# Optimization experiments

Measured on AMD Instinct MI355X. Metric: run time of the kernel, lower is better.

Reference implementation:

```python
import jax, jax.numpy as jnp
import numpy as np

WS = 512            # window_size
STEP = WS // 2      # hop
K = WS // 2 + 1     # rfft coeffs = 257


def hann(n):
    # periodic hann window (matches torch.hann_window default)
    return 0.5 * (1.0 - jnp.cos(2.0 * jnp.pi * jnp.arange(n) / n))


def setup_inputs() -> dict:
    key = jax.random.key(0)
    k1, k2, k3 = jax.random.split(key, 3)
    B, C, T = 4, 64, 65536
    x = jax.random.normal(k1, (B, C, T), dtype=jnp.float32)
    # mixer initialized near identity (nn.Parameter(torch.eye(C)) after some training)
    mixer = jnp.eye(C, dtype=jnp.float32) + 0.01 * jax.random.normal(k2, (C, C), dtype=jnp.float32)
    # stable per-coefficient transfer magnitudes in [0, 0.9)
    transfer = jax.random.uniform(k3, (C, K), dtype=jnp.float32) * 0.9
    gain = jnp.full((1,), 1.5, dtype=jnp.float32)
    return {"x": x, "mixer": mixer, "transfer": transfer, "gain": gain}


def reference(x, mixer, transfer, gain):
    B, C, T = x.shape
    # (x^T @ mixer)^T
    x = jnp.einsum('bct,cd->bdt', x, mixer)
    # windowed_audio: pad by hop, unfold into half-overlapping frames
    xp = jnp.pad(x, ((0, 0), (0, 0), (0, STEP)))
    n_frames = (xp.shape[-1] - WS) // STEP + 1
    idx = jnp.arange(n_frames)[:, None] * STEP + jnp.arange(WS)[None, :]  # [F, WS]
    windowed = xp[:, :, idx]                     # [B, C, F, WS]
    spec = jnp.fft.rfft(windowed, axis=-1)       # [B, C, F, K] complex64
    # linear recurrence over frames: y_i = (spec_i + y_{i-1}) * transfer
    def step(carry, s):
        y = (s + carry) * transfer[None]         # [B, C, K]
        return y, y
    spec_t = jnp.transpose(spec, (2, 0, 1, 3))   # [F, B, C, K]
    y0 = jnp.zeros((B, C, K), dtype=spec.dtype)
    _, ys = jax.lax.scan(step, y0, spec_t)       # [F, B, C, K]
    out_spec = jnp.transpose(ys, (1, 2, 0, 3))   # [B, C, F, K]
    # inverse FFT + windowed overlap-add
    aw = jnp.fft.irfft(out_spec, n=WS, axis=-1)  # [B, C, F, WS]
    aw = aw * hann(WS)[None, None, None, :]
    L = (n_frames - 1) * STEP + WS
    samples = jnp.zeros((B, C, L), dtype=aw.dtype).at[:, :, idx].add(aw)
    samples = jnp.tanh(samples * gain[0])
    return samples[..., :T]
```

## Files before the change

kernel.cpp:

```cpp
#include <hip/hip_runtime.h>
#include <math.h>

#define T_LEN  65536
#define T_PAD  65792
#define C_CH   64
#define STEP_  256
#define K_     257
#define NW     16
#define NIT    16
#define SPEC_ROW  257
#define SPEC_ROWF (2 * SPEC_ROW)

#define PIDX8(i) ((i) + (((i) >> 3) << 1))

#define WSYNC()  asm volatile("s_waitcnt lgkmcnt(0)" ::: "memory")
#define CFENCE() asm volatile("" ::: "memory")

__device__ __forceinline__ float2 cadd(float2 a, float2 b) { return make_float2(a.x + b.x, a.y + b.y); }
__device__ __forceinline__ float2 csub(float2 a, float2 b) { return make_float2(a.x - b.x, a.y - b.y); }
__device__ __forceinline__ float2 cmul(float2 a, float2 b) {
    return make_float2(a.x * b.x - a.y * b.y, a.x * b.y + a.y * b.x);
}
template <int SGN>
__device__ __forceinline__ float2 cmulsg(float2 w, float2 t) {
    if (SGN > 0) return make_float2(w.x * t.x - w.y * t.y, w.x * t.y + w.y * t.x);
    else         return make_float2(w.x * t.x + w.y * t.y, w.x * t.y - w.y * t.x);
}

template <int SGN>
__device__ __forceinline__ void bfly4(float2 z0, float2 z1, float2 z2, float2 z3,
                                      float2& o0, float2& o1, float2& o2, float2& o3,
                                      float2 w1, float2 w2, float2 w3) {
    float2 apc = cadd(z0, z2), amc = csub(z0, z2);
    float2 bpd = cadd(z1, z3), bmd = csub(z1, z3);
    float2 jb  = make_float2(-bmd.y, bmd.x);
    float2 t1, t3;
    if (SGN > 0) { t1 = csub(amc, jb); t3 = cadd(amc, jb); }
    else         { t1 = cadd(amc, jb); t3 = csub(amc, jb); }
    o0 = cadd(apc, bpd);
    o1 = cmulsg<SGN>(w1, t1);
    o2 = cmulsg<SGN>(w2, csub(apc, bpd));
    o3 = cmulsg<SGN>(w3, t3);
}
template <int SGN>
__device__ __forceinline__ void bfly4nt(float2 z0, float2 z1, float2 z2, float2 z3,
                                        float2& o0, float2& o1, float2& o2, float2& o3) {
    float2 apc = cadd(z0, z2), amc = csub(z0, z2);
    float2 bpd = cadd(z1, z3), bmd = csub(z1, z3);
    float2 jb  = make_float2(-bmd.y, bmd.x);
    o0 = cadd(apc, bpd);
    o2 = csub(apc, bpd);
    if (SGN > 0) { o1 = csub(amc, jb); o3 = cadd(amc, jb); }
    else         { o1 = cadd(amc, jb); o3 = csub(amc, jb); }
}

__device__ __forceinline__ float ftanh(float x) {
    float e = __expf(2.0f * x);
    return 1.0f - 2.0f * __builtin_amdgcn_rcpf(e + 1.0f);
}

__global__ __launch_bounds__(512, 1) void mix_kernel(const float* __restrict__ x,
                                                     const float* __restrict__ mixer,
                                                     float* __restrict__ mixed) {
    __shared__ __align__(16) float xt[64][128];
    __shared__ __align__(16) float mx[64][64];
    int tid = threadIdx.x;
    int b   = blockIdx.y;
    int t0  = blockIdx.x * 128;

    if (t0 >= T_LEN) {
        for (int f = tid; f < 8192; f += 512) {
            int d = f >> 7, tt = f & 127;
            mixed[((size_t)(b * C_CH + d)) * T_PAD + t0 + tt] = 0.0f;
        }
        return;
    }
    for (int f = tid; f < 4096; f += 512) reinterpret_cast<float*>(mx)[f] = mixer[f];
    for (int f4 = tid; f4 < 2048; f4 += 512) {
        int cc = f4 >> 5, tt4 = f4 & 31;
        *reinterpret_cast<float4*>(&xt[cc][tt4 * 4]) =
            *reinterpret_cast<const float4*>(&x[((size_t)(b * C_CH + cc)) * T_LEN + t0 + tt4 * 4]);
    }
    __syncthreads();

    int t = tid & 127, w = tid >> 7;
    int dbase = w * 16;
    float acc[16];
#pragma unroll
    for (int i = 0; i < 16; ++i) acc[i] = 0.0f;
    for (int cc = 0; cc < 64; ++cc) {
        float xv = xt[cc][t];
        float4 m0 = *reinterpret_cast<const float4*>(&mx[cc][dbase + 0]);
        float4 m1 = *reinterpret_cast<const float4*>(&mx[cc][dbase + 4]);
        float4 m2 = *reinterpret_cast<const float4*>(&mx[cc][dbase + 8]);
        float4 m3 = *reinterpret_cast<const float4*>(&mx[cc][dbase + 12]);
        acc[0]  = fmaf(xv, m0.x, acc[0]);  acc[1]  = fmaf(xv, m0.y, acc[1]);
        acc[2]  = fmaf(xv, m0.z, acc[2]);  acc[3]  = fmaf(xv, m0.w, acc[3]);
        acc[4]  = fmaf(xv, m1.x, acc[4]);  acc[5]  = fmaf(xv, m1.y, acc[5]);
        acc[6]  = fmaf(xv, m1.z, acc[6]);  acc[7]  = fmaf(xv, m1.w, acc[7]);
        acc[8]  = fmaf(xv, m2.x, acc[8]);  acc[9]  = fmaf(xv, m2.y, acc[9]);
        acc[10] = fmaf(xv, m2.z, acc[10]); acc[11] = fmaf(xv, m2.w, acc[11]);
        acc[12] = fmaf(xv, m3.x, acc[12]); acc[13] = fmaf(xv, m3.y, acc[13]);
        acc[14] = fmaf(xv, m3.z, acc[14]); acc[15] = fmaf(xv, m3.w, acc[15]);
    }
#pragma unroll
    for (int i = 0; i < 16; ++i)
        mixed[((size_t)(b * C_CH + dbase + i)) * T_PAD + t0 + t] = acc[i];
}

__global__ __launch_bounds__(1024) void stft_kernel(const float* __restrict__ mixed,
                                                    const float* __restrict__ transfer,
                                                    const float* __restrict__ gainp,
                                                    float* __restrict__ out) {
    __shared__ __align__(16) float2 buf[NW][320];
    __shared__ __align__(16) float2 spec[NW][SPEC_ROW];
    __shared__ __align__(16) float  olab[NW][264];
    __shared__ __align__(16) float  tails[2][264];

    const int tid  = threadIdx.x;
    const int bc   = blockIdx.x;
    const int b    = bc >> 6, c = bc & 63;
    const int g    = tid >> 6, lane = tid & 63;

    const float* src = mixed + ((size_t)(b * C_CH + c)) * T_PAD;
    float*       dst = out   + ((size_t)(b * C_CH + c)) * T_LEN;

    float2 pf0, pf1, pf2, pf3;
    {
        const float* fp = src + (size_t)g * STEP_;
        pf0 = *reinterpret_cast<const float2*>(fp + 2 * lane);
        pf1 = *reinterpret_cast<const float2*>(fp + 2 * (lane + 64));
        pf2 = *reinterpret_cast<const float2*>(fp + 2 * (lane + 128));
        pf3 = *reinterpret_cast<const float2*>(fp + 2 * (lane + 192));
    }

    const float TWO_PI = 6.2831853071795864f;
    float sn, cn;
    sincosf(TWO_PI * (float)lane / 256.0f, &sn, &cn);
    float2 w1a = make_float2(cn, -sn), w2a = cmul(w1a, w1a), w3a = cmul(w2a, w1a);
    sincosf(TWO_PI * (float)(lane >> 2) / 64.0f, &sn, &cn);
    float2 w1b = make_float2(cn, -sn), w2b = cmul(w1b, w1b), w3b = cmul(w2b, w1b);
    sincosf(TWO_PI * (float)(lane >> 4) / 16.0f, &sn, &cn);
    float2 w1c = make_float2(cn, -sn), w2c = cmul(w1c, w1c), w3c = cmul(w2c, w1c);
    float2 wh[4];
#pragma unroll
    for (int qq = 0; qq < 4; ++qq) {
        sincosf(3.14159265358979f * (float)(lane + 64 * qq) / 256.0f, &sn, &cn);
        wh[qq] = make_float2(cn, -sn);
    }
#define HV(m) ((0.5f - 0.5f * cosf(TWO_PI * (float)(m) / 512.0f)) * (1.0f / 512.0f))
    float h0 = HV(2 * lane),       h1 = HV(2 * lane + 1);
    float h2 = HV(2 * lane + 128), h3 = HV(2 * lane + 129);
    float h4 = HV(2 * lane + 256), h5 = HV(2 * lane + 257);
    float h6 = HV(2 * lane + 384), h7 = HV(2 * lane + 385);
#undef HV

    int se;
    if (lane < 32) se = (g << 5) | lane;
    else if (g == 0 && lane < 34) se = 480 + lane;
    else se = -1;
    float tcar = 0.0f, ycar = 0.0f;
    if (se >= 0) tcar = transfer[c * K_ + (se >> 1)];

    if (tid < 256) tails[0][tid] = 0.0f;
    const float gv = gainp[0];
    float2* bin = &buf[g][0];
    const int q2 = (lane & 3)  + ((lane >> 2) << 4);
    const int q3 = (lane & 15) + ((lane >> 4) << 6);
    __syncthreads();

    for (int it = 0; it < NIT; ++it) {
        const int f = it * NW + g;
        float2 z0 = pf0, z1 = pf1, z2 = pf2, z3 = pf3;
        if (it + 1 < NIT) {
            const float* fp = src + (size_t)(f + NW) * STEP_;
            pf0 = *reinterpret_cast<const float2*>(fp + 2 * lane);
            pf1 = *reinterpret_cast<const float2*>(fp + 2 * (lane + 64));
            pf2 = *reinterpret_cast<const float2*>(fp + 2 * (lane + 128));
            pf3 = *reinterpret_cast<const float2*>(fp + 2 * (lane + 192));
        }
        float2 o0, o1, o2, o3;
        bfly4<1>(z0, z1, z2, z3, o0, o1, o2, o3, w1a, w2a, w3a);
        {
            float2* bw = bin + PIDX8(4 * lane);
            *reinterpret_cast<float4*>(bw)     = make_float4(o0.x, o0.y, o1.x, o1.y);
            *reinterpret_cast<float4*>(bw + 2) = make_float4(o2.x, o2.y, o3.x, o3.y);
        }
        WSYNC();
        z0 = bin[PIDX8(lane)]; z1 = bin[PIDX8(lane + 64)];
        z2 = bin[PIDX8(lane + 128)]; z3 = bin[PIDX8(lane + 192)];
        bfly4<1>(z0, z1, z2, z3, o0, o1, o2, o3, w1b, w2b, w3b);
        CFENCE();
        bin[PIDX8(q2)] = o0; bin[PIDX8(q2 + 4)] = o1;
        bin[PIDX8(q2 + 8)] = o2; bin[PIDX8(q2 + 12)] = o3;
        WSYNC();
        z0 = bin[PIDX8(lane)]; z1 = bin[PIDX8(lane + 64)];
        z2 = bin[PIDX8(lane + 128)]; z3 = bin[PIDX8(lane + 192)];
        bfly4<1>(z0, z1, z2, z3, o0, o1, o2, o3, w1c, w2c, w3c);
        CFENCE();
        bin[PIDX8(q3)] = o0; bin[PIDX8(q3 + 16)] = o1;
        bin[PIDX8(q3 + 32)] = o2; bin[PIDX8(q3 + 48)] = o3;
        WSYNC();
        z0 = bin[PIDX8(lane)]; z1 = bin[PIDX8(lane + 64)];
        z2 = bin[PIDX8(lane + 128)]; z3 = bin[PIDX8(lane + 192)];
        bfly4nt<1>(z0, z1, z2, z3, o0, o1, o2, o3);
        CFENCE();
        bin[PIDX8(lane)] = o0; bin[PIDX8(lane + 64)] = o1;
        bin[PIDX8(lane + 128)] = o2; bin[PIDX8(lane + 192)] = o3;
        WSYNC();
#pragma unroll
        for (int qq = 0; qq < 4; ++qq) {
            int k = lane + 64 * qq;
            float2 u = bin[PIDX8(k)];
            float2 v = bin[PIDX8((256 - k) & 255)];
            float2 E = make_float2(0.5f * (u.x + v.x),  0.5f * (u.y - v.y));
            float2 O = make_float2(0.5f * (u.y + v.y), -0.5f * (u.x - v.x));
            spec[g][k] = cadd(E, cmul(wh[qq], O));
        }
        if (lane == 0) {
            float2 u0 = bin[PIDX8(0)];
            spec[g][256] = make_float2(u0.x - u0.y, 0.0f);
        }
        __syncthreads();
        if (se >= 0) {
            float* sf = reinterpret_cast<float*>(&spec[0][0]);
            float y = ycar;
#pragma unroll
            for (int gg = 0; gg < NW; ++gg) {
                float vv = sf[gg * SPEC_ROWF + se];
                y = (vv + y) * tcar;
                sf[gg * SPEC_ROWF + se] = y;
            }
            ycar = y;
        }
        __syncthreads();
        {
            float2 zz[4];
#pragma unroll
            for (int qq = 0; qq < 4; ++qq) {
                int k = lane + 64 * qq;
                float2 u  = spec[g][k];
                float2 s2 = spec[g][256 - k];
                float2 A  = make_float2(u.x + s2.x, u.y - s2.y);
                float2 D  = make_float2(u.x - s2.x, u.y + s2.y);
                float2 Bv = cmulsg<-1>(wh[qq], D);
                zz[qq] = make_float2(A.x - Bv.y, A.y + Bv.x);
            }
            bfly4<-1>(zz[0], zz[1], zz[2], zz[3], o0, o1, o2, o3, w1a, w2a, w3a);
        }
        {
            float2* bw = bin + PIDX8(4 * lane);
            *reinterpret_cast<float4*>(bw)     = make_float4(o0.x, o0.y, o1.x, o1.y);
            *reinterpret_cast<float4*>(bw + 2) = make_float4(o2.x, o2.y, o3.x, o3.y);
        }
        WSYNC();
        z0 = bin[PIDX8(lane)]; z1 = bin[PIDX8(lane + 64)];
        z2 = bin[PIDX8(lane + 128)]; z3 = bin[PIDX8(lane + 192)];
        bfly4<-1>(z0, z1, z2, z3, o0, o1, o2, o3, w1b, w2b, w3b);
        CFENCE();
        bin[PIDX8(q2)] = o0; bin[PIDX8(q2 + 4)] = o1;
        bin[PIDX8(q2 + 8)] = o2; bin[PIDX8(q2 + 12)] = o3;
        WSYNC();
        z0 = bin[PIDX8(lane)]; z1 = bin[PIDX8(lane + 64)];
        z2 = bin[PIDX8(lane + 128)]; z3 = bin[PIDX8(lane + 192)];
        bfly4<-1>(z0, z1, z2, z3, o0, o1, o2, o3, w1c, w2c, w3c);
        CFENCE();
        bin[PIDX8(q3)] = o0; bin[PIDX8(q3 + 16)] = o1;
        bin[PIDX8(q3 + 32)] = o2; bin[PIDX8(q3 + 48)] = o3;
        WSYNC();
        z0 = bin[PIDX8(lane)]; z1 = bin[PIDX8(lane + 64)];
        z2 = bin[PIDX8(lane + 128)]; z3 = bin[PIDX8(lane + 192)];
        bfly4nt<-1>(z0, z1, z2, z3, o0, o1, o2, o3);
        {
            float2 sh0 = make_float2(o2.x * h4, o2.y * h5);
            float2 sh1 = make_float2(o3.x * h6, o3.y * h7);
            float* wrow = (g == NW - 1) ? tails[(it + 1) & 1] : olab[g + 1];
            *reinterpret_cast<float2*>(&wrow[2 * lane])       = sh0;
            *reinterpret_cast<float2*>(&wrow[2 * lane + 128]) = sh1;
        }
        __syncthreads();
        {
            const float* prow = (g == 0) ? tails[it & 1] : olab[g];
            float2 p0 = *reinterpret_cast<const float2*>(&prow[2 * lane]);
            float2 p1 = *reinterpret_cast<const float2*>(&prow[2 * lane + 128]);
            float2 r0 = make_float2(ftanh((o0.x * h0 + p0.x) * gv),
                                    ftanh((o0.y * h1 + p0.y) * gv));
            float2 r1 = make_float2(ftanh((o1.x * h2 + p1.x) * gv),
                                    ftanh((o1.y * h3 + p1.y) * gv));
            float* dp = dst + (size_t)f * STEP_;
            *reinterpret_cast<float2*>(&dp[2 * lane])       = r0;
            *reinterpret_cast<float2*>(&dp[2 * lane + 128]) = r1;
        }
    }
}

extern "C" void kernel_launch(void* const* d_in, const int* in_sizes, int n_in,
                              void* d_out, int out_size, void* d_ws, size_t ws_size,
                              hipStream_t stream) {
    (void)in_sizes; (void)n_in; (void)out_size; (void)ws_size;
    const float* x        = (const float*)d_in[0];
    const float* mixer    = (const float*)d_in[1];
    const float* transfer = (const float*)d_in[2];
    const float* gain     = (const float*)d_in[3];
    float* out   = (float*)d_out;
    float* mixed = (float*)d_ws;

    dim3 gmix(T_PAD / 128, 4);
    mix_kernel<<<gmix, 512, 0, stream>>>(x, mixer, mixed);
    stft_kernel<<<256, 1024, 0, stream>>>(mixed, transfer, gain, out);
}
```

Baseline: 124.3 us.

## Software-pipeline STFT forward/inverse FFT across iterations with double-buffered spectrum

Restructures the stft loop so the forward FFT of frame group it overlaps with the inverse FFT of group it-1, using a double-buffered spec array. This cuts the barriers per iteration from three to two. LDS padding is replaced by an XOR swizzle, and the intra-wave s_waitcnt syncs between FFT stages are dropped in favour of compiler fences only. The recurrence is reassigned to 8 full wavefronts, and the mix kernel now computes two time samples per thread with float2 stores. The risks are intra-wave LDS ordering correctness after removing the waitcnts, and more LDS use per block.

```diff
diff --git a/kernel.cpp b/kernel.cpp
--- a/kernel.cpp
+++ b/kernel.cpp
@@ -8,13 +8,14 @@
 #define K_     257
 #define NW     16
 #define NIT    16
-#define SPEC_ROW  257
-#define SPEC_ROWF (2 * SPEC_ROW)
-
-#define PIDX8(i) ((i) + (((i) >> 3) << 1))
-
-#define WSYNC()  asm volatile("s_waitcnt lgkmcnt(0)" ::: "memory")
+#define SPEC_ROWF 514
+
+#define SW(i) ((i) ^ (((i) >> 2) & 12))
+
 #define CFENCE() asm volatile("" ::: "memory")
+#define BAR() do { asm volatile("s_waitcnt lgkmcnt(0)" ::: "memory"); \
+                   __builtin_amdgcn_s_barrier(); \
+                   asm volatile("" ::: "memory"); } while (0)
 
 __device__ __forceinline__ float2 cadd(float2 a, float2 b) { return make_float2(a.x + b.x, a.y + b.y); }
 __device__ __forceinline__ float2 csub(float2 a, float2 b) { return make_float2(a.x - b.x, a.y - b.y); }
@@ -26,7 +27,6 @@
     if (SGN > 0) return make_float2(w.x * t.x - w.y * t.y, w.x * t.y + w.y * t.x);
     else         return make_float2(w.x * t.x + w.y * t.y, w.x * t.y - w.y * t.x);
 }
-
 template <int SGN>
 __device__ __forceinline__ void bfly4(float2 z0, float2 z1, float2 z2, float2 z3,
                                       float2& o0, float2& o1, float2& o2, float2& o3,
@@ -83,37 +83,35 @@
     }
     __syncthreads();
 
-    int t = tid & 127, w = tid >> 7;
-    int dbase = w * 16;
-    float acc[16];
-#pragma unroll
-    for (int i = 0; i < 16; ++i) acc[i] = 0.0f;
+    int tp = tid & 63, grp = tid >> 6;
+    int dbase = grp * 8;
+    float2 acc[8];
+#pragma unroll
+    for (int i = 0; i < 8; ++i) acc[i] = make_float2(0.0f, 0.0f);
     for (int cc = 0; cc < 64; ++cc) {
-        float xv = xt[cc][t];
+        float2 xv = *reinterpret_cast<const float2*>(&xt[cc][2 * tp]);
         float4 m0 = *reinterpret_cast<const float4*>(&mx[cc][dbase + 0]);
         float4 m1 = *reinterpret_cast<const float4*>(&mx[cc][dbase + 4]);
-        float4 m2 = *reinterpret_cast<const float4*>(&mx[cc][dbase + 8]);
-        float4 m3 = *reinterpret_cast<const float4*>(&mx[cc][dbase + 12]);
-        acc[0]  = fmaf(xv, m0.x, acc[0]);  acc[1]  = fmaf(xv, m0.y, acc[1]);
-        acc[2]  = fmaf(xv, m0.z, acc[2]);  acc[3]  = fmaf(xv, m0.w, acc[3]);
-        acc[4]  = fmaf(xv, m1.x, acc[4]);  acc[5]  = fmaf(xv, m1.y, acc[5]);
-        acc[6]  = fmaf(xv, m1.z, acc[6]);  acc[7]  = fmaf(xv, m1.w, acc[7]);
-        acc[8]  = fmaf(xv, m2.x, acc[8]);  acc[9]  = fmaf(xv, m2.y, acc[9]);
-        acc[10] = fmaf(xv, m2.z, acc[10]); acc[11] = fmaf(xv, m2.w, acc[11]);
-        acc[12] = fmaf(xv, m3.x, acc[12]); acc[13] = fmaf(xv, m3.y, acc[13]);
-        acc[14] = fmaf(xv, m3.z, acc[14]); acc[15] = fmaf(xv, m3.w, acc[15]);
-    }
-#pragma unroll
-    for (int i = 0; i < 16; ++i)
-        mixed[((size_t)(b * C_CH + dbase + i)) * T_PAD + t0 + t] = acc[i];
+        acc[0].x = fmaf(xv.x, m0.x, acc[0].x); acc[0].y = fmaf(xv.y, m0.x, acc[0].y);
+        acc[1].x = fmaf(xv.x, m0.y, acc[1].x); acc[1].y = fmaf(xv.y, m0.y, acc[1].y);
+        acc[2].x = fmaf(xv.x, m0.z, acc[2].x); acc[2].y = fmaf(xv.y, m0.z, acc[2].y);
+        acc[3].x = fmaf(xv.x, m0.w, acc[3].x); acc[3].y = fmaf(xv.y, m0.w, acc[3].y);
+        acc[4].x = fmaf(xv.x, m1.x, acc[4].x); acc[4].y = fmaf(xv.y, m1.x, acc[4].y);
+        acc[5].x = fmaf(xv.x, m1.y, acc[5].x); acc[5].y = fmaf(xv.y, m1.y, acc[5].y);
+        acc[6].x = fmaf(xv.x, m1.z, acc[6].x); acc[6].y = fmaf(xv.y, m1.z, acc[6].y);
+        acc[7].x = fmaf(xv.x, m1.w, acc[7].x); acc[7].y = fmaf(xv.y, m1.w, acc[7].y);
+    }
+#pragma unroll
+    for (int i = 0; i < 8; ++i)
+        *reinterpret_cast<float2*>(&mixed[((size_t)(b * C_CH + dbase + i)) * T_PAD + t0 + 2 * tp]) = acc[i];
 }
 
 __global__ __launch_bounds__(1024) void stft_kernel(const float* __restrict__ mixed,
                                                     const float* __restrict__ transfer,
                                                     const float* __restrict__ gainp,
                                                     float* __restrict__ out) {
-    __shared__ __align__(16) float2 buf[NW][320];
-    __shared__ __align__(16) float2 spec[NW][SPEC_ROW];
+    __shared__ __align__(16) float2 buf[NW][256];
+    __shared__ __align__(16) float2 spec[2][NW][257];
     __shared__ __align__(16) float  olab[NW][264];
     __shared__ __align__(16) float  tails[2][264];
 
@@ -155,141 +153,146 @@
     float h6 = HV(2 * lane + 384), h7 = HV(2 * lane + 385);
 #undef HV
 
-    int se;
-    if (lane < 32) se = (g << 5) | lane;
-    else if (g == 0 && lane < 34) se = 480 + lane;
-    else se = -1;
+    int se = -1;
+    if (g < 8) se = (g << 6) | lane;
+    else if (g == 8 && lane < 2) se = 512 + lane;
     float tcar = 0.0f, ycar = 0.0f;
     if (se >= 0) tcar = transfer[c * K_ + (se >> 1)];
 
     if (tid < 256) tails[0][tid] = 0.0f;
     const float gv = gainp[0];
     float2* bin = &buf[g][0];
-    const int q2 = (lane & 3)  + ((lane >> 2) << 4);
-    const int q3 = (lane & 15) + ((lane >> 4) << 6);
-    __syncthreads();
-
-    for (int it = 0; it < NIT; ++it) {
-        const int f = it * NW + g;
-        float2 z0 = pf0, z1 = pf1, z2 = pf2, z3 = pf3;
-        if (it + 1 < NIT) {
-            const float* fp = src + (size_t)(f + NW) * STEP_;
-            pf0 = *reinterpret_cast<const float2*>(fp + 2 * lane);
-            pf1 = *reinterpret_cast<const float2*>(fp + 2 * (lane + 64));
-            pf2 = *reinterpret_cast<const float2*>(fp + 2 * (lane + 128));
-            pf3 = *reinterpret_cast<const float2*>(fp + 2 * (lane + 192));
+    const int q2  = (lane & 3)  + ((lane >> 2) << 4);
+    const int q3  = (lane & 15) + ((lane >> 4) << 6);
+    const int s1b = (4 * lane) ^ (lane & 12);
+    BAR();
+
+    for (int it = 0; it <= NIT; ++it) {
+        const int sp = it & 1, sp2 = sp ^ 1;
+        if (it < NIT) {
+            const int f = it * NW + g;
+            float2 z0 = pf0, z1 = pf1, z2 = pf2, z3 = pf3;
+            if (it + 1 < NIT) {
+                const float* fp = src + (size_t)(f + NW) * STEP_;
+                pf0 = *reinterpret_cast<const float2*>(fp + 2 * lane);
+                pf1 = *reinterpret_cast<const float2*>(fp + 2 * (lane + 64));
+                pf2 = *reinterpret_cast<const float2*>(fp + 2 * (lane + 128));
+                pf3 = *reinterpret_cast<const float2*>(fp + 2 * (lane + 192));
+            }
+            float2 o0, o1, o2, o3;
+            bfly4<1>(z0, z1, z2, z3, o0, o1, o2, o3, w1a, w2a, w3a);
+            {
+                float2* bw = bin + s1b;
+                *reinterpret_cast<float4*>(bw)     = make_float4(o0.x, o0.y, o1.x, o1.y);
+                *reinterpret_cast<float4*>(bw + 2) = make_float4(o2.x, o2.y, o3.x, o3.y);
+            }
+            CFENCE();
+            z0 = bin[SW(lane)]; z1 = bin[SW(lane + 64)];
+            z2 = bin[SW(lane + 128)]; z3 = bin[SW(lane + 192)];
+            bfly4<1>(z0, z1, z2, z3, o0, o1, o2, o3, w1b, w2b, w3b);
+            CFENCE();
+            bin[SW(q2)] = o0; bin[SW(q2 + 4)] = o1;
+            bin[SW(q2 + 8)] = o2; bin[SW(q2 + 12)] = o3;
+            CFENCE();
+            z0 = bin[SW(lane)]; z1 = bin[SW(lane + 64)];
+            z2 = bin[SW(lane + 128)]; z3 = bin[SW(lane + 192)];
+            bfly4<1>(z0, z1, z2, z3, o0, o1, o2, o3, w1c, w2c, w3c);
+            CFENCE();
+            bin[SW(q3)] = o0; bin[SW(q3 + 16)] = o1;
+            bin[SW(q3 + 32)] = o2; bin[SW(q3 + 48)] = o3;
+            CFENCE();
+            z0 = bin[SW(lane)]; z1 = bin[SW(lane + 64)];
+            z2 = bin[SW(lane + 128)]; z3 = bin[SW(lane + 192)];
+            bfly4nt<1>(z0, z1, z2, z3, o0, o1, o2, o3);
+            CFENCE();
+            bin[SW(lane)] = o0; bin[SW(lane + 64)] = o1;
+            bin[SW(lane + 128)] = o2; bin[SW(lane + 192)] = o3;
+            CFENCE();
+#pragma unroll
+            for (int qq = 0; qq < 4; ++qq) {
+                int k = lane + 64 * qq;
+                float2 u = bin[SW(k)];
+                float2 v = bin[SW((256 - k) & 255)];
+                float2 E = make_float2(0.5f * (u.x + v.x),  0.5f * (u.y - v.y));
+                float2 O = make_float2(0.5f * (u.y + v.y), -0.5f * (u.x - v.x));
+                spec[sp][g][k] = cadd(E, cmul(wh[qq], O));
+            }
+            if (lane == 0) {
+                float2 u0 = bin[SW(0)];
+                spec[sp][g][256] = make_float2(u0.x - u0.y, 0.0f);
+            }
         }
-        float2 o0, o1, o2, o3;
-        bfly4<1>(z0, z1, z2, z3, o0, o1, o2, o3, w1a, w2a, w3a);
-        {
-            float2* bw = bin + PIDX8(4 * lane);
-            *reinterpret_cast<float4*>(bw)     = make_float4(o0.x, o0.y, o1.x, o1.y);
-            *reinterpret_cast<float4*>(bw + 2) = make_float4(o2.x, o2.y, o3.x, o3.y);
-        }
-        WSYNC();
-        z0 = bin[PIDX8(lane)]; z1 = bin[PIDX8(lane + 64)];
-        z2 = bin[PIDX8(lane + 128)]; z3 = bin[PIDX8(lane + 192)];
-        bfly4<1>(z0, z1, z2, z3, o0, o1, o2, o3, w1b, w2b, w3b);
-        CFENCE();
-        bin[PIDX8(q2)] = o0; bin[PIDX8(q2 + 4)] = o1;
-        bin[PIDX8(q2 + 8)] = o2; bin[PIDX8(q2 + 12)] = o3;
-        WSYNC();
-        z0 = bin[PIDX8(lane)]; z1 = bin[PIDX8(lane + 64)];
-        z2 = bin[PIDX8(lane + 128)]; z3 = bin[PIDX8(lane + 192)];
-        bfly4<1>(z0, z1, z2, z3, o0, o1, o2, o3, w1c, w2c, w3c);
-        CFENCE();
-        bin[PIDX8(q3)] = o0; bin[PIDX8(q3 + 16)] = o1;
-        bin[PIDX8(q3 + 32)] = o2; bin[PIDX8(q3 + 48)] = o3;
-        WSYNC();
-        z0 = bin[PIDX8(lane)]; z1 = bin[PIDX8(lane + 64)];
-        z2 = bin[PIDX8(lane + 128)]; z3 = bin[PIDX8(lane + 192)];
-        bfly4nt<1>(z0, z1, z2, z3, o0, o1, o2, o3);
-        CFENCE();
-        bin[PIDX8(lane)] = o0; bin[PIDX8(lane + 64)] = o1;
-        bin[PIDX8(lane + 128)] = o2; bin[PIDX8(lane + 192)] = o3;
-        WSYNC();
-#pragma unroll
-        for (int qq = 0; qq < 4; ++qq) {
-            int k = lane + 64 * qq;
-            float2 u = bin[PIDX8(k)];
-            float2 v = bin[PIDX8((256 - k) & 255)];
-            float2 E = make_float2(0.5f * (u.x + v.x),  0.5f * (u.y - v.y));
-            float2 O = make_float2(0.5f * (u.y + v.y), -0.5f * (u.x - v.x));
-            spec[g][k] = cadd(E, cmul(wh[qq], O));
-        }
-        if (lane == 0) {
-            float2 u0 = bin[PIDX8(0)];
-            spec[g][256] = make_float2(u0.x - u0.y, 0.0f);
-        }
-        __syncthreads();
-        if (se >= 0) {
-            float* sf = reinterpret_cast<float*>(&spec[0][0]);
+        BAR();
+        if (it < NIT && se >= 0) {
+            float* sf = reinterpret_cast<float*>(&spec[sp][0][0]);
             float y = ycar;
 #pragma unroll
             for (int gg = 0; gg < NW; ++gg) {
-                float vv = sf[gg * SPEC_ROWF + se];
-                y = (vv + y) * tcar;
+                y = (sf[gg * SPEC_ROWF + se] + y) * tcar;
                 sf[gg * SPEC_ROWF + se] = y;
             }
             ycar = y;
         }
-        __syncthreads();
-        {
-            float2 zz[4];
-#pragma unroll
-            for (int qq = 0; qq < 4; ++qq) {
-                int k = lane + 64 * qq;
-                float2 u  = spec[g][k];
-                float2 s2 = spec[g][256 - k];
-                float2 A  = make_float2(u.x + s2.x, u.y - s2.y);
-                float2 D  = make_float2(u.x - s2.x, u.y + s2.y);
-                float2 Bv = cmulsg<-1>(wh[qq], D);
-                zz[qq] = make_float2(A.x - Bv.y, A.y + Bv.x);
-            }
-            bfly4<-1>(zz[0], zz[1], zz[2], zz[3], o0, o1, o2, o3, w1a, w2a, w3a);
-        }
-        {
-            float2* bw = bin + PIDX8(4 * lane);
-            *reinterpret_cast<float4*>(bw)     = make_float4(o0.x, o0.y, o1.x, o1.y);
-            *reinterpret_cast<float4*>(bw + 2) = make_float4(o2.x, o2.y, o3.x, o3.y);
-        }
-        WSYNC();
-        z0 = bin[PIDX8(lane)]; z1 = bin[PIDX8(lane + 64)];
-        z2 = bin[PIDX8(lane + 128)]; z3 = bin[PIDX8(lane + 192)];
-        bfly4<-1>(z0, z1, z2, z3, o0, o1, o2, o3, w1b, w2b, w3b);
-        CFENCE();
-        bin[PIDX8(q2)] = o0; bin[PIDX8(q2 + 4)] = o1;
-        bin[PIDX8(q2 + 8)] = o2; bin[PIDX8(q2 + 12)] = o3;
-        WSYNC();
-        z0 = bin[PIDX8(lane)]; z1 = bin[PIDX8(lane + 64)];
-        z2 = bin[PIDX8(lane + 128)]; z3 = bin[PIDX8(lane + 192)];
-        bfly4<-1>(z0, z1, z2, z3, o0, o1, o2, o3, w1c, w2c, w3c);
-        CFENCE();
-        bin[PIDX8(q3)] = o0; bin[PIDX8(q3 + 16)] = o1;
-        bin[PIDX8(q3 + 32)] = o2; bin[PIDX8(q3 + 48)] = o3;
-        WSYNC();
-        z0 = bin[PIDX8(lane)]; z1 = bin[PIDX8(lane + 64)];
-        z2 = bin[PIDX8(lane + 128)]; z3 = bin[PIDX8(lane + 192)];
-        bfly4nt<-1>(z0, z1, z2, z3, o0, o1, o2, o3);
-        {
-            float2 sh0 = make_float2(o2.x * h4, o2.y * h5);
-            float2 sh1 = make_float2(o3.x * h6, o3.y * h7);
-            float* wrow = (g == NW - 1) ? tails[(it + 1) & 1] : olab[g + 1];
-            *reinterpret_cast<float2*>(&wrow[2 * lane])       = sh0;
-            *reinterpret_cast<float2*>(&wrow[2 * lane + 128]) = sh1;
-        }
-        __syncthreads();
-        {
-            const float* prow = (g == 0) ? tails[it & 1] : olab[g];
-            float2 p0 = *reinterpret_cast<const float2*>(&prow[2 * lane]);
-            float2 p1 = *reinterpret_cast<const float2*>(&prow[2 * lane + 128]);
-            float2 r0 = make_float2(ftanh((o0.x * h0 + p0.x) * gv),
-                                    ftanh((o0.y * h1 + p0.y) * gv));
-            float2 r1 = make_float2(ftanh((o1.x * h2 + p1.x) * gv),
-                                    ftanh((o1.y * h3 + p1.y) * gv));
-            float* dp = dst + (size_t)f * STEP_;
-            *reinterpret_cast<float2*>(&dp[2 * lane])       = r0;
-            *reinterpret_cast<float2*>(&dp[2 * lane + 128]) = r1;
+        if (it > 0) {
+            const int fb = (it - 1) * NW + g;
+            float2 o0, o1, o2, o3;
+            {
+                float2 zz[4];
+#pragma unroll
+                for (int qq = 0; qq < 4; ++qq) {
+                    int k = lane + 64 * qq;
+                    float2 u  = spec[sp2][g][k];
+                    float2 s2 = spec[sp2][g][256 - k];
+                    float2 A  = make_float2(u.x + s2.x, u.y - s2.y);
+                    float2 D  = make_float2(u.x - s2.x, u.y + s2.y);
+                    float2 Bv = cmulsg<-1>(wh[qq], D);
+                    zz[qq] = make_float2(A.x - Bv.y, A.y + Bv.x);
+                }
+                bfly4<-1>(zz[0], zz[1], zz[2], zz[3], o0, o1, o2, o3, w1a, w2a, w3a);
+            }
+            {
+                float2* bw = bin + s1b;
+                *reinterpret_cast<float4*>(bw)     = make_float4(o0.x, o0.y, o1.x, o1.y);
+                *reinterpret_cast<float4*>(bw + 2) = make_float4(o2.x, o2.y, o3.x, o3.y);
+            }
+            CFENCE();
+            float2 z0 = bin[SW(lane)], z1 = bin[SW(lane + 64)];
+            float2 z2 = bin[SW(lane + 128)], z3 = bin[SW(lane + 192)];
+            bfly4<-1>(z0, z1, z2, z3, o0, o1, o2, o3, w1b, w2b, w3b);
+            CFENCE();
+            bin[SW(q2)] = o0; bin[SW(q2 + 4)] = o1;
+            bin[SW(q2 + 8)] = o2; bin[SW(q2 + 12)] = o3;
+            CFENCE();
+            z0 = bin[SW(lane)]; z1 = bin[SW(lane + 64)];
+            z2 = bin[SW(lane + 128)]; z3 = bin[SW(lane + 192)];
+            bfly4<-1>(z0, z1, z2, z3, o0, o1, o2, o3, w1c, w2c, w3c);
+            CFENCE();
+            bin[SW(q3)] = o0; bin[SW(q3 + 16)] = o1;
+            bin[SW(q3 + 32)] = o2; bin[SW(q3 + 48)] = o3;
+            CFENCE();
+            z0 = bin[SW(lane)]; z1 = bin[SW(lane + 64)];
+            z2 = bin[SW(lane + 128)]; z3 = bin[SW(lane + 192)];
+            bfly4nt<-1>(z0, z1, z2, z3, o0, o1, o2, o3);
+            {
+                float2 sh0 = make_float2(o2.x * h4, o2.y * h5);
+                float2 sh1 = make_float2(o3.x * h6, o3.y * h7);
+                float* wrow = (g == NW - 1) ? tails[it & 1] : olab[g + 1];
+                *reinterpret_cast<float2*>(&wrow[2 * lane])       = sh0;
+                *reinterpret_cast<float2*>(&wrow[2 * lane + 128]) = sh1;
+            }
+            BAR();
+            {
+                const float* prow = (g == 0) ? tails[(it - 1) & 1] : olab[g];
+                float2 p0 = *reinterpret_cast<const float2*>(&prow[2 * lane]);
+                float2 p1 = *reinterpret_cast<const float2*>(&prow[2 * lane + 128]);
+                float2 r0 = make_float2(ftanh((o0.x * h0 + p0.x) * gv),
+                                        ftanh((o0.y * h1 + p0.y) * gv));
+                float2 r1 = make_float2(ftanh((o1.x * h2 + p1.x) * gv),
+                                        ftanh((o1.y * h3 + p1.y) * gv));
+                float* dp = dst + (size_t)fb * STEP_;
+                *reinterpret_cast<float2*>(&dp[2 * lane])       = r0;
+                *reinterpret_cast<float2*>(&dp[2 * lane + 128]) = r1;
+            }
         }
     }
 }
```

Result: faster. 113.5 us (-8.7%).
